# Kernel optimization log

Hardware: AMD Instinct MI355X
Metric: run time of the kernel (lower is better)

The kernel has to match this reference:

```python
import jax, jax.numpy as jnp
import numpy as np
from jax.scipy.special import erf

F = 64          # scalar feature channels (hidden_irreps multiplicity)
S = 9           # spherical harmonics dim for max_ell=2
NB = 8          # num_bessel
RMAX = 5.0
PPOLY = 5       # num_polynomial_cutoff
AVG_NEIGH = 16.0
SIGMA = 1.0     # atomic_multipoles_smearing_width
KE = 1.0        # Coulomb constant (model units)
N = 20000; G = 20; E = 320000; NEL = 10; L = 2; HMLP = 16

def _sph_l2(u):
    # real spherical harmonics up to l=2, e3nn 'component' normalization,
    # with permute_to_e3nn_convention (y, z, x) ordering for l=1
    x, y, z = u[..., 0], u[..., 1], u[..., 2]
    s3 = 1.7320508075688772; s5 = 2.23606797749979; s15 = 3.872983346207417
    return jnp.stack([jnp.ones_like(x),
                      s3 * y, s3 * z, s3 * x,
                      s15 * x * y, s15 * y * z, 0.5 * s5 * (3.0 * z * z - 1.0),
                      s15 * x * z, 0.5 * s15 * (x * x - y * y)], axis=-1)

def _radial(r):
    # Bessel basis with smooth polynomial cutoff (p = PPOLY)
    n = jnp.arange(1, NB + 1, dtype=r.dtype)
    rb = jnp.sqrt(2.0 / RMAX) * jnp.sin(n * jnp.pi * r[:, None] / RMAX) / r[:, None]
    x = r / RMAX
    p = float(PPOLY)
    u = (1.0 - 0.5 * (p + 1.0) * (p + 2.0) * x**PPOLY
         + p * (p + 2.0) * x**(PPOLY + 1) - 0.5 * p * (p + 1.0) * x**(PPOLY + 2))
    u = jnp.where(x < 1.0, u, 0.0)
    return rb * u[:, None]

def setup_inputs() -> dict:
    key = jax.random.key(0)
    ks = jax.random.split(key, 20)
    Ng = N // G
    species = jax.random.randint(ks[0], (N,), 0, NEL)
    node_attrs = jax.nn.one_hot(species, NEL, dtype=jnp.float32)
    positions = jax.random.uniform(ks[1], (N, 3), dtype=jnp.float32) * 10.0
    g = jax.random.randint(ks[2], (E,), 0, G)
    s_loc = jax.random.randint(ks[3], (E,), 0, Ng)
    off = jax.random.randint(ks[4], (E,), 1, Ng)   # avoid self edges
    r_loc = (s_loc + off) % Ng
    edge_index = jnp.stack([g * Ng + s_loc, g * Ng + r_loc], axis=0)
    batch = jnp.repeat(jnp.arange(G), Ng)
    sc = 0.1
    atomic_energies = jax.random.normal(ks[5], (NEL,)) * sc
    embed_w = jax.random.normal(ks[6], (NEL, F)) * sc
    radial_w1 = jax.random.normal(ks[7], (L, NB, 64)) * 0.3
    radial_b1 = jnp.zeros((L, 64), jnp.float32)
    radial_w2 = jax.random.normal(ks[8], (L, 64, F)) * 0.2
    prod_w = jax.random.normal(ks[9], (L, NEL, F)) * 0.3
    readout_w = jax.random.normal(ks[10], (L, F)) * sc
    ro2_w1 = jax.random.normal(ks[11], (F, HMLP)) * 0.2
    ro2_b1 = jnp.zeros((HMLP,), jnp.float32)
    ro2_w2 = jax.random.normal(ks[12], (HMLP, 1)) * 0.2
    charge_w = jax.random.normal(ks[13], (L, F)) * sc
    flux_w = jax.random.normal(ks[14], (L, NB)) * sc
    formal_charges = jax.random.normal(ks[15], (NEL,)) * 0.5
    return dict(node_attrs=node_attrs, positions=positions, edge_index=edge_index,
                batch=batch, num_graphs=G, atomic_energies=atomic_energies,
                embed_w=embed_w, radial_w1=radial_w1, radial_b1=radial_b1,
                radial_w2=radial_w2, prod_w=prod_w, readout_w=readout_w,
                ro2_w1=ro2_w1, ro2_b1=ro2_b1, ro2_w2=ro2_w2,
                charge_w=charge_w, flux_w=flux_w, formal_charges=formal_charges)

def reference(node_attrs, positions, edge_index, batch, num_graphs,
              atomic_energies, embed_w, radial_w1, radial_b1, radial_w2,
              prod_w, readout_w, ro2_w1, ro2_b1, ro2_w2,
              charge_w, flux_w, formal_charges):
    Nn = node_attrs.shape[0]
    Ng = Nn // num_graphs
    snd, rcv = edge_index[0], edge_index[1]
    # atomic reference energies (E0) and node embedding
    node_e0 = node_attrs @ atomic_energies                      # [N]
    e0 = jax.ops.segment_sum(node_e0, batch, num_graphs)        # [G]
    node_scalars = node_attrs @ embed_w                         # [N,F]
    # edge geometry: gather, spherical harmonics, radial embedding
    vec = positions[rcv] - positions[snd]                       # [E,3]
    lengths = jnp.sqrt((vec * vec).sum(-1) + 1e-12)             # [E]
    unit = vec / lengths[:, None]
    edge_attrs = _sph_l2(unit)                                  # [E,S]
    edge_feats = _radial(lengths)                               # [E,NB]
    # formal charges (per-species)
    FQ = node_attrs @ formal_charges                            # [N]
    charge_density = FQ
    flux = jnp.zeros_like(lengths)
    energies = [e0]
    node_e_list = [node_e0]
    nL = radial_w1.shape[0]
    for l in range(nL):
        # interaction: radial MLP -> per-edge TP messages -> scatter sum
        R = jax.nn.silu(edge_feats @ radial_w1[l] + radial_b1[l]) @ radial_w2[l]  # [E,F]
        m = (R * node_scalars[snd])[:, :, None] * edge_attrs[:, None, :]          # [E,F,S]
        agg = jax.ops.segment_sum(m, rcv, Nn) / AVG_NEIGH                         # [N,F,S]
        # equivariant product (correlation-2 flavor) + element-dependent skip
        sk = node_scalars * (node_attrs @ prod_w[l])                              # [N,F]
        feats = agg + agg * agg[:, :, :1]                                         # [N,F,S]
        node_scalars = feats[:, :, 0] + sk                                        # [N,F]
        if l == nL - 1:
            node_energies = (jax.nn.silu(node_scalars @ ro2_w1 + ro2_b1) @ ro2_w2)[:, 0]
        else:
            node_energies = node_scalars @ readout_w[l]
        energies.append(jax.ops.segment_sum(node_energies, batch, num_graphs))
        node_e_list.append(node_energies)
        # long-range source maps: per-node charge + per-edge flux contributions
        charge_density = charge_density + node_scalars @ charge_w[l]
        flux = flux + edge_feats @ flux_w[l]
    contributions = jnp.stack(energies, -1)                     # [G, L+1]
    total_energy = contributions.sum(-1)                        # [G]
    node_energy = jnp.stack(node_e_list, -1).sum(-1)            # [N]
    # polarization: edge-flux dipole + formal-charge dipole
    pol = jax.ops.segment_sum(flux[:, None] * vec, batch[rcv], num_graphs)
    pol = pol + jax.ops.segment_sum(FQ[:, None] * positions, batch, num_graphs)
    # direct (non-PBC) screened Coulomb energy per graph, equal-size graphs
    q = charge_density.reshape(num_graphs, Ng)
    p = positions.reshape(num_graphs, Ng, 3)
    d = p[:, :, None, :] - p[:, None, :, :]
    r = jnp.sqrt((d * d).sum(-1) + 1e-12)
    kern = erf(r / (2.0 * SIGMA)) / r * (1.0 - jnp.eye(Ng, dtype=r.dtype))
    e_el = 0.5 * KE * jnp.einsum('gi,gij,gj->g', q, kern, q)
    total_energy = total_energy + e_el
    total_charge = jax.ops.segment_sum(charge_density, batch, num_graphs)
    return total_energy, node_energy, contributions, pol, total_charge
```

## Files before the change

kernel.cpp:

```cpp
#include <hip/hip_runtime.h>
#include <math.h>

#define NEL 10
#define FD 64
#define NBES 8
#define GG 20
#define HML 16
#define EGB 512
#define NUB 5000

typedef __attribute__((ext_vector_type(8))) short short8;
typedef __attribute__((ext_vector_type(4))) float f32x4;

__device__ __forceinline__ float wred(float v) {
    #pragma unroll
    for (int off = 32; off > 0; off >>= 1) v += __shfl_down(v, off, 64);
    return v;
}

__device__ __forceinline__ float silu(float h) {
    return h / (1.f + __expf(-h));
}

__device__ __forceinline__ unsigned short f2bf(float x) {
    unsigned int b = __float_as_uint(x);
    unsigned int r = (b + 0x7FFFu + ((b >> 16) & 1u)) >> 16;
    return (unsigned short)r;
}

__device__ __forceinline__ int xcd_swizzle(int bid, int nb) {
    int q = nb >> 3, r = nb & 7;
    int x = bid & 7, i = bid >> 3;
    return (x < r ? x * (q + 1) : r * (q + 1) + (x - r) * q) + i;
}

__global__ __launch_bounds__(256) void setup_k(
    const float* __restrict__ attrs, const float* __restrict__ ae,
    const float* __restrict__ fc, const float* __restrict__ embed_w,
    const int* __restrict__ eidx, int* __restrict__ spec,
    float* __restrict__ q, float* __restrict__ out,
    float* __restrict__ scal, float* __restrict__ agg0,
    int* __restrict__ cnt,
    const float* __restrict__ w1, const float* __restrict__ w2,
    unsigned short* __restrict__ w1bf, unsigned short* __restrict__ w2bf,
    int N_, int E_)
{
    int idx = blockIdx.x * 256 + threadIdx.x;
    int lane = threadIdx.x & 63;
    int n = idx >> 6;
    bool pred = (lane < NEL) && (attrs[(size_t)n * NEL + lane] > 0.5f);
    unsigned long long m = __ballot(pred);
    int sp = (int)__builtin_ctzll(m);
    scal[idx] = embed_w[sp * FD + lane];
    agg0[idx] = 0.f;
    if (lane == 0) { spec[n] = sp; q[n] = fc[sp]; out[GG + n] = ae[sp]; }
    if (idx < E_) atomicAdd(&cnt[eidx[E_ + idx]], 1);
    if (idx < GG) out[idx] = 0.f;
    if (idx < 8192) {
        int l = idx >> 12, rem = idx & 4095;
        int f = rem >> 6, k = rem & 63;
        w2bf[idx] = f2bf(w2[l * 4096 + k * 64 + f]);
    } else if (idx < 9216) {
        int j = idx - 8192;
        int l = j >> 9, rem = j & 511;
        int mm = rem >> 3, jj = rem & 7;
        w1bf[j] = f2bf(w1[l * 512 + jj * 64 + mm]);
    }
}

__global__ __launch_bounds__(1024) void scan_k(
    const int* __restrict__ cnt, int* __restrict__ cur, int N_)
{
    int t = threadIdx.x;
    __shared__ int wtot[16];
    int lane = t & 63, wid = t >> 6;
    int base = t * 20;
    int c[20]; int s = 0;
    bool full = (base + 20 <= N_);
    if (full) {
        #pragma unroll
        for (int i = 0; i < 5; ++i) {
            int4 v4 = *(const int4*)&cnt[base + i * 4];
            c[i*4+0] = v4.x; c[i*4+1] = v4.y; c[i*4+2] = v4.z; c[i*4+3] = v4.w;
        }
        #pragma unroll
        for (int i = 0; i < 20; ++i) s += c[i];
    } else {
        #pragma unroll
        for (int i = 0; i < 20; ++i) { int idx = base + i; c[i] = (idx < N_) ? cnt[idx] : 0; s += c[i]; }
    }
    int v = s;
    #pragma unroll
    for (int off = 1; off < 64; off <<= 1) {
        int u = __shfl_up(v, off, 64);
        if (lane >= off) v += u;
    }
    if (lane == 63) wtot[wid] = v;
    __syncthreads();
    if (wid == 0 && lane < 16) {
        int wv = wtot[lane];
        #pragma unroll
        for (int off = 1; off < 16; off <<= 1) {
            int u = __shfl_up(wv, off, 64);
            if (lane >= off) wv += u;
        }
        wtot[lane] = wv;
    }
    __syncthreads();
    int ex = (wid > 0 ? wtot[wid - 1] : 0) + (v - s);
    if (full) {
        int o[20];
        #pragma unroll
        for (int i = 0; i < 20; ++i) { o[i] = ex; ex += c[i]; }
        #pragma unroll
        for (int i = 0; i < 5; ++i)
            *(int4*)&cur[base + i * 4] = make_int4(o[i*4+0], o[i*4+1], o[i*4+2], o[i*4+3]);
    } else {
        #pragma unroll
        for (int i = 0; i < 20; ++i) {
            int idx = base + i;
            if (idx < N_) { cur[idx] = ex; ex += c[i]; }
        }
    }
}

__global__ __launch_bounds__(256) void geom_scatter_k(
    const float* __restrict__ pos, const int* __restrict__ eidx,
    const float* __restrict__ flux_w, int* __restrict__ cur,
    unsigned int* __restrict__ esd, float* __restrict__ polpart,
    int E_, int ng)
{
    __shared__ float lpol[GG * 3];
    int tid = threadIdx.x;
    for (int i = tid; i < GG * 3; i += 256) lpol[i] = 0.f;
    __syncthreads();
    float fw[NBES];
    #pragma unroll
    for (int i = 0; i < NBES; ++i) fw[i] = flux_w[i] + flux_w[NBES + i];
    const float PI = 3.14159265358979323846f;
    for (int e = blockIdx.x * 256 + tid; e < E_; e += EGB * 256) {
        int s = eidx[e], r = eidx[E_ + e];
        float dx = pos[(size_t)r*3+0] - pos[(size_t)s*3+0];
        float dy = pos[(size_t)r*3+1] - pos[(size_t)s*3+1];
        float dz = pos[(size_t)r*3+2] - pos[(size_t)s*3+2];
        float len = sqrtf(dx*dx + dy*dy + dz*dz + 1e-12f);
        float x = len * 0.2f;
        float u = 0.f;
        if (x < 1.f) {
            float x2 = x * x;
            float x5 = x2 * x2 * x;
            u = 1.f - 21.f * x5 + 35.f * x5 * x - 15.f * x5 * x2;
        }
        float pref = 0.6324555320336759f / len * u;
        float theta = PI * x;
        float s1, c1;
        __sincosf(theta, &s1, &c1);
        float c2 = 2.f * c1;
        float sp_ = 0.f, sn = s1;
        float flux = 0.f;
        unsigned int pk[4];
        #pragma unroll
        for (int i = 0; i < 4; ++i) {
            float r0 = pref * sn;
            float n1 = c2 * sn - sp_; sp_ = sn; sn = n1;
            float r1 = pref * sn;
            n1 = c2 * sn - sp_; sp_ = sn; sn = n1;
            flux += r0 * fw[2*i] + r1 * fw[2*i+1];
            pk[i] = (unsigned int)f2bf(r0) | ((unsigned int)f2bf(r1) << 16);
        }
        int p = atomicAdd(&cur[r], 1);
        size_t off = (size_t)p * 8;
        *(uint4*)&esd[off]     = make_uint4(pk[0], pk[1], pk[2], pk[3]);
        *(uint2*)&esd[off + 4] = make_uint2((unsigned int)s, (unsigned int)r);
        int g = r / ng;
        atomicAdd(&lpol[g*3+0], flux * dx);
        atomicAdd(&lpol[g*3+1], flux * dy);
        atomicAdd(&lpol[g*3+2], flux * dz);
    }
    __syncthreads();
    for (int i = tid; i < GG * 3; i += 256) polpart[blockIdx.x * (GG * 3) + i] = lpol[i];
}

__global__ __launch_bounds__(256, 4) void edge_mlp_k(
    const unsigned int* __restrict__ esd,
    const unsigned short* __restrict__ w1bf, const float* __restrict__ b1,
    const unsigned short* __restrict__ w2bf, const float* __restrict__ scal,
    float* __restrict__ agg0, int layer, int E_)
{
    __shared__ __align__(16) char smem[4][4352];
    int t = threadIdx.x, w = t >> 6, lane = t & 63;
    int mrow = lane & 15, quad = lane >> 4;
    int xb = xcd_swizzle(blockIdx.x, gridDim.x);
    int wbase = (xb * 4 + w) * 64;
    unsigned short* hw = (unsigned short*)smem[w];
    float* cw = (float*)smem[w];

    const short8 z8 = {0,0,0,0,0,0,0,0};
    short8 a1f[4];
    #pragma unroll
    for (int nt = 0; nt < 4; ++nt) {
        a1f[nt] = z8;
        if (quad == 0) a1f[nt] = *(const short8*)&w1bf[layer * 512 + (nt * 16 + mrow) * 8];
        else if (quad == 1) a1f[nt][0] = (short)f2bf(b1[layer * FD + nt * 16 + mrow]);
    }
    const unsigned short* wb = w2bf + layer * 4096;
    short8 bf0[4], bf1[4];
    #pragma unroll
    for (int nt = 0; nt < 4; ++nt) {
        bf0[nt] = *(const short8*)&wb[(nt * 16 + mrow) * 64 + quad * 8];
        bf1[nt] = *(const short8*)&wb[(nt * 16 + mrow) * 64 + 32 + quad * 8];
    }

    f32x4 zf = {0.f, 0.f, 0.f, 0.f};
    int curR = -1;
    float run = 0.f;

    #pragma unroll 1
    for (int grp = 0; grp < 4; ++grp) {
        int ebase = wbase + grp * 16;
        int2 sr = *(const int2*)&esd[(size_t)(ebase + mrow) * 8 + 4];
        int sv = sr.x, rv = sr.y;
        if (grp == 0) curR = __builtin_amdgcn_readlane(rv, 0);

        short8 b_ef = z8;
        if (quad == 0) b_ef = *(const short8*)&esd[(size_t)(ebase + mrow) * 8];
        else if (quad == 1) b_ef[0] = (short)0x3F80;

        #pragma unroll
        for (int nt = 0; nt < 4; ++nt) {
            f32x4 c1 = __builtin_amdgcn_mfma_f32_16x16x32_bf16(a1f[nt], b_ef, zf, 0, 0, 0);
            unsigned int p01 = (unsigned int)f2bf(silu(c1[0])) | ((unsigned int)f2bf(silu(c1[1])) << 16);
            unsigned int p23 = (unsigned int)f2bf(silu(c1[2])) | ((unsigned int)f2bf(silu(c1[3])) << 16);
            *(uint2*)&hw[mrow * 72 + nt * 16 + quad * 4] = make_uint2(p01, p23);
        }

        short8 a0  = *(const short8*)&hw[mrow * 72 + quad * 8];
        short8 a1b = *(const short8*)&hw[mrow * 72 + 32 + quad * 8];
        f32x4 c[4];
        #pragma unroll
        for (int nt = 0; nt < 4; ++nt) {
            f32x4 cc = __builtin_amdgcn_mfma_f32_16x16x32_bf16(a0, bf0[nt], zf, 0, 0, 0);
            cc = __builtin_amdgcn_mfma_f32_16x16x32_bf16(a1b, bf1[nt], cc, 0, 0, 0);
            c[nt] = cc;
        }
        #pragma unroll
        for (int nt = 0; nt < 4; ++nt)
            #pragma unroll
            for (int reg = 0; reg < 4; ++reg)
                cw[(quad * 4 + reg) * 68 + nt * 16 + mrow] = c[nt][reg];

        #pragma unroll
        for (int half = 0; half < 2; ++half) {
            float cv[8], sw[8];
            #pragma unroll
            for (int k = 0; k < 8; ++k) {
                int pp = half * 8 + k;
                cv[k] = cw[pp * 68 + lane];
                int s = __builtin_amdgcn_readlane(sv, pp);
                sw[k] = scal[(size_t)s * FD + lane];
            }
            #pragma unroll
            for (int k = 0; k < 8; ++k) {
                int pp = half * 8 + k;
                int r = __builtin_amdgcn_readlane(rv, pp);
                float v = cv[k] * sw[k];
                if (r != curR) {
                    atomicAdd(&agg0[(size_t)curR * FD + lane], run);
                    run = v; curR = r;
                } else {
                    run += v;
                }
            }
        }
    }
    atomicAdd(&agg0[(size_t)curR * FD + lane], run);
}

__global__ __launch_bounds__(256) void node_update_k(
    float* __restrict__ scal, float* __restrict__ agg0,
    const int* __restrict__ spec, const float* __restrict__ prod_w,
    const float* __restrict__ readout_w, const float* __restrict__ ro2_w1,
    const float* __restrict__ ro2_b1, const float* __restrict__ ro2_w2,
    const float* __restrict__ charge_w, float* __restrict__ q,
    float* __restrict__ out_nodeE, float* __restrict__ nEpart,
    int layer, int last, int N_)
{
    __shared__ float vsh[4][FD];
    __shared__ float red[4];
    int wid = threadIdx.x >> 6, lane = threadIdx.x & 63;
    int n = blockIdx.x * 4 + wid;
    int sp = spec[n];
    size_t idx = (size_t)n * FD + lane;
    float a = agg0[idx] * 0.0625f;
    if (!last) agg0[idx] = 0.f;
    float v = a + a * a + scal[idx] * prod_w[(layer * NEL + sp) * FD + lane];
    scal[idx] = v;

    float ne;
    if (!last) {
        ne = wred(v * readout_w[layer * FD + lane]);
    } else {
        vsh[wid][lane] = v;
        float h = 0.f;
        if (lane < HML) {
            h = ro2_b1[lane];
            for (int ff = 0; ff < FD; ++ff) h += vsh[wid][ff] * ro2_w1[ff * HML + lane];
            h = silu(h) * ro2_w2[lane];
        }
        ne = wred(h);
    }
    float qs = wred(v * charge_w[layer * FD + lane]);
    if (lane == 0) {
        out_nodeE[n] += ne;
        q[n] += qs;
        red[wid] = ne;
    }
    __syncthreads();
    if (threadIdx.x == 0) nEpart[layer * NUB + blockIdx.x] = red[0] + red[1] + red[2] + red[3];
}

__global__ __launch_bounds__(256) void coulomb_final_k(
    const float* __restrict__ q, const float* __restrict__ pos,
    const int* __restrict__ spec, const float* __restrict__ ae,
    const float* __restrict__ fc, const float* __restrict__ nEpart,
    const float* __restrict__ polpart, float* __restrict__ out,
    int N_, int ng)
{
    __shared__ float sh[260];
    int vb = blockIdx.x;
    int g = vb / 137, rem = vb % 137;
    int t = threadIdx.x, lane = t & 63, w = t >> 6;

    if (rem < 136) {
        int a = 0, r2 = rem;
        while (r2 >= 16 - a) { r2 -= 16 - a; ++a; }
        int b = a + r2;
        const float* qg = q + (size_t)g * ng;
        const float* pg = pos + (size_t)g * ng * 3;
        float* qs_ = sh; float* jx = sh + 64; float* jy = sh + 128; float* jz = sh + 192;
        if (t < 64) {
            int j = b * 64 + t;
            bool ok = j < ng;
            qs_[t] = ok ? qg[j] : 0.f;
            jx[t] = ok ? pg[(size_t)j*3+0] : 0.f;
            jy[t] = ok ? pg[(size_t)j*3+1] : 0.f;
            jz[t] = ok ? pg[(size_t)j*3+2] : 0.f;
        }
        __syncthreads();
        int i = a * 64 + lane;
        float accu = 0.f;
        if (i < ng) {
            float qi = qg[i];
            float xi = pg[(size_t)i*3+0], yi = pg[(size_t)i*3+1], zi = pg[(size_t)i*3+2];
            #pragma unroll 4
            for (int k = 0; k < 16; ++k) {
                int jj = w * 16 + k;
                int j = b * 64 + jj;
                float dx = xi - jx[jj], dy = yi - jy[jj], dz = zi - jz[jj];
                float d2 = dx*dx + dy*dy + dz*dz + 1e-12f;
                float rinv = __frsqrt_rn(d2);
                float r = d2 * rinv;
                float x = 0.5f * r;
                float tt = __frcp_rn(1.f + 0.3275911f * x);
                float poly = ((((1.061405429f*tt - 1.453152027f)*tt + 1.421413741f)*tt
                               - 0.284496736f)*tt + 0.254829592f)*tt;
                float erfv = 1.f - poly * __expf(-x * x);
                float kern = (j == i) ? 0.f : erfv * rinv;
                accu += qi * qs_[jj] * kern;
            }
        }
        accu = wred(accu);
        if (lane == 0) sh[256 + w] = accu;
        __syncthreads();
        if (t == 0) {
            float s = sh[256] + sh[257] + sh[258] + sh[259];
            atomicAdd(&out[g], (a == b) ? 0.5f * s : s);
        }
    } else {
        float se0 = 0.f, sq = 0.f, p0 = 0.f, p1 = 0.f, p2 = 0.f, s0 = 0.f, s1 = 0.f;
        for (int n = g * ng + t; n < (g + 1) * ng; n += 256) {
            int sp = spec[n];
            float fq = fc[sp];
            se0 += ae[sp];
            sq += q[n];
            p0 += fq * pos[(size_t)n*3+0];
            p1 += fq * pos[(size_t)n*3+1];
            p2 += fq * pos[(size_t)n*3+2];
        }
        if (t < 250) {
            int b = g * 250 + t;
            s0 = nEpart[b];
            s1 = nEpart[NUB + b];
        }
        for (int b = t; b < EGB; b += 256) {
            p0 += polpart[b * (GG * 3) + g * 3 + 0];
            p1 += polpart[b * (GG * 3) + g * 3 + 1];
            p2 += polpart[b * (GG * 3) + g * 3 + 2];
        }
        float vals[7] = {se0, s0, s1, sq, p0, p1, p2};
        float* red = sh;
        #pragma unroll
        for (int k = 0; k < 7; ++k) {
            float r = wred(vals[k]);
            if (lane == 0) red[w * 8 + k] = r;
        }
        __syncthreads();
        if (t < 7) sh[64 + t] = red[t] + red[8 + t] + red[16 + t] + red[24 + t];
        __syncthreads();
        if (t == 0) {
            float a0 = sh[64], a1 = sh[65], a2 = sh[66];
            atomicAdd(&out[g], a0 + a1 + a2);
            float* contrib = out + GG + N_;
            contrib[g*3+0] = a0; contrib[g*3+1] = a1; contrib[g*3+2] = a2;
            float* pol = contrib + GG * 3;
            pol[g*3+0] = sh[68]; pol[g*3+1] = sh[69]; pol[g*3+2] = sh[70];
            float* qt = pol + GG * 3;
            qt[g] = sh[67];
        }
    }
}

extern "C" void kernel_launch(void* const* d_in, const int* in_sizes, int n_in,
                              void* d_out, int out_size, void* d_ws, size_t ws_size,
                              hipStream_t stream)
{
    const float* node_attrs      = (const float*)d_in[0];
    const float* positions       = (const float*)d_in[1];
    const int*   edge_index      = (const int*)d_in[2];
    const float* atomic_energies = (const float*)d_in[5];
    const float* embed_w         = (const float*)d_in[6];
    const float* radial_w1       = (const float*)d_in[7];
    const float* radial_b1       = (const float*)d_in[8];
    const float* radial_w2       = (const float*)d_in[9];
    const float* prod_w          = (const float*)d_in[10];
    const float* readout_w       = (const float*)d_in[11];
    const float* ro2_w1          = (const float*)d_in[12];
    const float* ro2_b1          = (const float*)d_in[13];
    const float* ro2_w2          = (const float*)d_in[14];
    const float* charge_w        = (const float*)d_in[15];
    const float* flux_w          = (const float*)d_in[16];
    const float* formal_charges  = (const float*)d_in[17];

    int N = in_sizes[0] / NEL;
    int E = in_sizes[2] / 2;
    int ng = N / GG;

    float* ws      = (float*)d_ws;
    float* scal    = ws;
    float* agg0    = scal + (size_t)N * FD;
    unsigned int* esd = (unsigned int*)(agg0 + (size_t)N * FD);
    float* q       = (float*)(esd + (size_t)E * 8);
    int*   spec    = (int*)(q + N);
    float* nEpart  = (float*)(spec + N);
    float* polpart = nEpart + 2 * NUB;
    int*   cnt     = (int*)(polpart + EGB * (GG * 3));
    int*   cur     = cnt + N;
    unsigned short* w2bf = (unsigned short*)(cur + N);
    unsigned short* w1bf = w2bf + 8192;

    float* out = (float*)d_out;
    float* out_nodeE = out + GG;

    hipMemsetAsync(cnt, 0, (size_t)N * sizeof(int), stream);

    setup_k<<<(N * FD) / 256, 256, 0, stream>>>(
        node_attrs, atomic_energies, formal_charges, embed_w, edge_index,
        spec, q, out, scal, agg0, cnt, radial_w1, radial_w2, w1bf, w2bf, N, E);
    scan_k<<<1, 1024, 0, stream>>>(cnt, cur, N);
    geom_scatter_k<<<EGB, 256, 0, stream>>>(
        positions, edge_index, flux_w, cur, esd, polpart, E, ng);

    for (int l = 0; l < 2; ++l) {
        edge_mlp_k<<<E / 256, 256, 0, stream>>>(
            esd, w1bf, radial_b1, w2bf, scal, agg0, l, E);
        node_update_k<<<N / 4, 256, 0, stream>>>(
            scal, agg0, spec, prod_w, readout_w, ro2_w1, ro2_b1, ro2_w2,
            charge_w, q, out_nodeE, nEpart, l, (l == 1) ? 1 : 0, N);
    }

    coulomb_final_k<<<GG * 137, 256, 0, stream>>>(
        q, positions, spec, atomic_energies, formal_charges,
        nEpart, polpart, out, N, ng);
}
```

Measured before the change: 263.5 us.

## Split edge records into packed bessel and id arrays, store uncontended segments

```diff
diff --git a/kernel.cpp b/kernel.cpp
--- a/kernel.cpp
+++ b/kernel.cpp
@@ -39,7 +39,7 @@
     const float* __restrict__ fc, const float* __restrict__ embed_w,
     const int* __restrict__ eidx, int* __restrict__ spec,
     float* __restrict__ q, float* __restrict__ out,
-    float* __restrict__ scal, float* __restrict__ agg0,
+    float* __restrict__ scal,
     int* __restrict__ cnt,
     const float* __restrict__ w1, const float* __restrict__ w2,
     unsigned short* __restrict__ w1bf, unsigned short* __restrict__ w2bf,
@@ -52,7 +52,6 @@
     unsigned long long m = __ballot(pred);
     int sp = (int)__builtin_ctzll(m);
     scal[idx] = embed_w[sp * FD + lane];
-    agg0[idx] = 0.f;
     if (lane == 0) { spec[n] = sp; q[n] = fc[sp]; out[GG + n] = ae[sp]; }
     if (idx < E_) atomicAdd(&cnt[eidx[E_ + idx]], 1);
     if (idx < GG) out[idx] = 0.f;
@@ -127,8 +126,8 @@
 __global__ __launch_bounds__(256) void geom_scatter_k(
     const float* __restrict__ pos, const int* __restrict__ eidx,
     const float* __restrict__ flux_w, int* __restrict__ cur,
-    unsigned int* __restrict__ esd, float* __restrict__ polpart,
-    int E_, int ng)
+    unsigned short* __restrict__ bessel, unsigned int* __restrict__ ids,
+    float* __restrict__ polpart, int E_, int ng)
 {
     __shared__ float lpol[GG * 3];
     int tid = threadIdx.x;
@@ -169,9 +168,8 @@
             pk[i] = (unsigned int)f2bf(r0) | ((unsigned int)f2bf(r1) << 16);
         }
         int p = atomicAdd(&cur[r], 1);
-        size_t off = (size_t)p * 8;
-        *(uint4*)&esd[off]     = make_uint4(pk[0], pk[1], pk[2], pk[3]);
-        *(uint2*)&esd[off + 4] = make_uint2((unsigned int)s, (unsigned int)r);
+        *(uint4*)&bessel[(size_t)p * NBES] = make_uint4(pk[0], pk[1], pk[2], pk[3]);
+        ids[p] = (unsigned int)s | ((unsigned int)r << 16);
         int g = r / ng;
         atomicAdd(&lpol[g*3+0], flux * dx);
         atomicAdd(&lpol[g*3+1], flux * dy);
@@ -182,7 +180,7 @@
 }
 
 __global__ __launch_bounds__(256, 4) void edge_mlp_k(
-    const unsigned int* __restrict__ esd,
+    const unsigned short* __restrict__ bessel, const unsigned int* __restrict__ ids,
     const unsigned short* __restrict__ w1bf, const float* __restrict__ b1,
     const unsigned short* __restrict__ w2bf, const float* __restrict__ scal,
     float* __restrict__ agg0, int layer, int E_)
@@ -195,6 +193,9 @@
     unsigned short* hw = (unsigned short*)smem[w];
     float* cw = (float*)smem[w];
 
+    unsigned int ids_all = ids[wbase + lane];
+    int firstR = (int)(__builtin_amdgcn_readlane(ids_all, 0) >> 16);
+
     const short8 z8 = {0,0,0,0,0,0,0,0};
     short8 a1f[4];
     #pragma unroll
@@ -212,18 +213,15 @@
     }
 
     f32x4 zf = {0.f, 0.f, 0.f, 0.f};
-    int curR = -1;
+    int curR = firstR;
     float run = 0.f;
 
     #pragma unroll 1
     for (int grp = 0; grp < 4; ++grp) {
         int ebase = wbase + grp * 16;
-        int2 sr = *(const int2*)&esd[(size_t)(ebase + mrow) * 8 + 4];
-        int sv = sr.x, rv = sr.y;
-        if (grp == 0) curR = __builtin_amdgcn_readlane(rv, 0);
 
         short8 b_ef = z8;
-        if (quad == 0) b_ef = *(const short8*)&esd[(size_t)(ebase + mrow) * 8];
+        if (quad == 0) b_ef = *(const short8*)&bessel[(size_t)(ebase + mrow) * NBES];
         else if (quad == 1) b_ef[0] = (short)0x3F80;
 
         #pragma unroll
@@ -252,20 +250,22 @@
         #pragma unroll
         for (int half = 0; half < 2; ++half) {
             float cv[8], sw[8];
+            unsigned int idv[8];
             #pragma unroll
             for (int k = 0; k < 8; ++k) {
                 int pp = half * 8 + k;
                 cv[k] = cw[pp * 68 + lane];
-                int s = __builtin_amdgcn_readlane(sv, pp);
-                sw[k] = scal[(size_t)s * FD + lane];
+                idv[k] = __builtin_amdgcn_readlane(ids_all, grp * 16 + pp);
+                sw[k] = scal[(size_t)(idv[k] & 0xffffu) * FD + lane];
             }
             #pragma unroll
             for (int k = 0; k < 8; ++k) {
-                int pp = half * 8 + k;
-                int r = __builtin_amdgcn_readlane(rv, pp);
+                int r = (int)(idv[k] >> 16);
                 float v = cv[k] * sw[k];
                 if (r != curR) {
-                    atomicAdd(&agg0[(size_t)curR * FD + lane], run);
+                    float* dst = &agg0[(size_t)curR * FD + lane];
+                    if (curR != firstR) *dst = run;
+                    else atomicAdd(dst, run);
                     run = v; curR = r;
                 } else {
                     run += v;
@@ -448,31 +448,32 @@
     float* ws      = (float*)d_ws;
     float* scal    = ws;
     float* agg0    = scal + (size_t)N * FD;
-    unsigned int* esd = (unsigned int*)(agg0 + (size_t)N * FD);
-    float* q       = (float*)(esd + (size_t)E * 8);
+    int*   cnt     = (int*)(agg0 + (size_t)N * FD);
+    int*   cur     = cnt + N;
+    unsigned short* bessel = (unsigned short*)(cur + N);
+    unsigned int*   ids    = (unsigned int*)(bessel + (size_t)E * NBES);
+    float* q       = (float*)(ids + E);
     int*   spec    = (int*)(q + N);
     float* nEpart  = (float*)(spec + N);
     float* polpart = nEpart + 2 * NUB;
-    int*   cnt     = (int*)(polpart + EGB * (GG * 3));
-    int*   cur     = cnt + N;
-    unsigned short* w2bf = (unsigned short*)(cur + N);
+    unsigned short* w2bf = (unsigned short*)(polpart + EGB * (GG * 3));
     unsigned short* w1bf = w2bf + 8192;
 
     float* out = (float*)d_out;
     float* out_nodeE = out + GG;
 
-    hipMemsetAsync(cnt, 0, (size_t)N * sizeof(int), stream);
+    hipMemsetAsync(agg0, 0, ((size_t)N * FD + N) * sizeof(float), stream);
 
     setup_k<<<(N * FD) / 256, 256, 0, stream>>>(
         node_attrs, atomic_energies, formal_charges, embed_w, edge_index,
-        spec, q, out, scal, agg0, cnt, radial_w1, radial_w2, w1bf, w2bf, N, E);
+        spec, q, out, scal, cnt, radial_w1, radial_w2, w1bf, w2bf, N, E);
     scan_k<<<1, 1024, 0, stream>>>(cnt, cur, N);
     geom_scatter_k<<<EGB, 256, 0, stream>>>(
-        positions, edge_index, flux_w, cur, esd, polpart, E, ng);
+        positions, edge_index, flux_w, cur, bessel, ids, polpart, E, ng);
 
     for (int l = 0; l < 2; ++l) {
         edge_mlp_k<<<E / 256, 256, 0, stream>>>(
-            esd, w1bf, radial_b1, w2bf, scal, agg0, l, E);
+            bessel, ids, w1bf, radial_b1, w2bf, scal, agg0, l, E);
         node_update_k<<<N / 4, 256, 0, stream>>>(
             scal, agg0, spec, prod_w, readout_w, ro2_w1, ro2_b1, ro2_w2,
             charge_w, q, out_nodeE, nEpart, l, (l == 1) ? 1 : 0, N);
```

Measured after the change: 253.6 us. -3.8%, faster.
